# Performance work log

Hardware: AMD Instinct MI355X
Metric: run time of the kernel (lower is better)

Reference implementation:

```python
import jax, jax.numpy as jnp
import numpy as np

N = 100_000   # nodes
E = 1_600_000 # edges
G, H1, H2, Z = 64, 64, 64, 32


def _w(k, o, i):
    return jax.random.normal(k, (o, i), jnp.float32) * (1.0 / np.sqrt(i))


def setup_inputs() -> dict:
    key = jax.random.key(0)
    ks = jax.random.split(key, 16)
    inp = {
        "x": jax.random.normal(ks[0], (N, G), jnp.float32),
        "edge_src": jax.random.randint(ks[1], (E,), 0, N, jnp.int32),
        "edge_dst": jax.random.randint(ks[2], (E,), 0, N, jnp.int32),
        "eps": jax.random.normal(ks[3], (N, Z), jnp.float32),
        "W1": _w(ks[4], H1, G),  "b1": jnp.zeros((H1,), jnp.float32),
        "W2": _w(ks[5], H2, H1), "b2": jnp.zeros((H2,), jnp.float32),
        "W31": _w(ks[6], Z, H2), "b31": jnp.zeros((Z,), jnp.float32),
        "W32": _w(ks[7], Z, H2), "b32": jnp.zeros((Z,), jnp.float32),
        "W4": _w(ks[8], H2, Z),  "b4": jnp.zeros((H2,), jnp.float32),
        "W5": _w(ks[9], H1, H2), "b5": jnp.zeros((H1,), jnp.float32),
        "W6": _w(ks[10], G, H1), "b6": jnp.zeros((G,), jnp.float32),
    }
    return inp


def _gcn(h, W, b, act, src, dst, norm):
    # message: h_src * norm_src, gathered per edge  [E, d]
    m = (h * norm)[src]
    # reduce: sum over incoming edges, scaled by norm_dst  [N, d]
    agg = jax.ops.segment_sum(m, dst, num_segments=N) * norm
    # node apply: linear + activation
    return act(agg @ W.T + b)


def reference(x, edge_src, edge_dst, eps,
              W1, b1, W2, b2, W31, b31, W32, b32, W4, b4, W5, b5, W6, b6):
    # symmetric GCN norm: deg^{-1/2} from in-degree
    deg = jax.ops.segment_sum(jnp.ones((E,), jnp.float32), edge_dst, num_segments=N)
    norm = jax.lax.rsqrt(jnp.maximum(deg, 1.0))[:, None]  # [N,1]

    relu = jax.nn.relu
    ident = lambda h: h

    h = _gcn(x, W1, b1, relu, edge_src, edge_dst, norm)
    h = _gcn(h, W2, b2, relu, edge_src, edge_dst, norm)
    mu = _gcn(h, W31, b31, ident, edge_src, edge_dst, norm)
    log_var = _gcn(h, W32, b32, ident, edge_src, edge_dst, norm)

    z = eps * jnp.exp(0.5 * log_var) + mu

    h = _gcn(z, W4, b4, relu, edge_src, edge_dst, norm)
    h = _gcn(h, W5, b5, relu, edge_src, edge_dst, norm)
    recon = _gcn(h, W6, b6, jax.nn.sigmoid, edge_src, edge_dst, norm)
    return recon, mu, log_var
```

## Files before the change

### kernel.cpp

```cpp
#include <hip/hip_runtime.h>
#include <hip/hip_fp16.h>
#include <math.h>

#define NN 100000
#define NE 1600000
#define NBKT 391
#define CHUNK 8192
#define NB1 ((NE + CHUNK - 1) / CHUNK)
#define QSEG 25000
#define NNP (NN + 8)

typedef _Float16 v8h __attribute__((ext_vector_type(8)));
typedef float v4f __attribute__((ext_vector_type(4)));

__global__ __launch_bounds__(256) void p0_hist_kernel(const int* __restrict__ dst,
                                                      int* __restrict__ bcnt) {
    __shared__ int h[NBKT];
    for (int b = threadIdx.x; b < NBKT; b += 256) h[b] = 0;
    __syncthreads();
    int e0 = blockIdx.x * CHUNK;
    for (int k = 0; k < CHUNK / 256; ++k) {
        int e = e0 + threadIdx.x + k * 256;
        if (e < NE) atomicAdd(&h[dst[e] >> 8], 1);
    }
    __syncthreads();
    for (int b = threadIdx.x; b < NBKT; b += 256)
        if (h[b]) atomicAdd(&bcnt[b], h[b]);
}

__global__ void scan_buckets_kernel(const int* __restrict__ bcnt, int* __restrict__ bbase,
                                    int* __restrict__ bcur) {
    __shared__ int s[512];
    int tid = threadIdx.x;
    int v = (tid < NBKT) ? bcnt[tid] : 0;
    s[tid] = v;
    __syncthreads();
    for (int off = 1; off < 512; off <<= 1) {
        int t = (tid >= off) ? s[tid - off] : 0;
        __syncthreads();
        s[tid] += t;
        __syncthreads();
    }
    if (tid < NBKT) { int ex = s[tid] - v; bbase[tid] = ex; bcur[tid] = ex; }
    if (tid == NBKT) bbase[NBKT] = NE;
}

__global__ __launch_bounds__(256) void p1_scatter_kernel(const int* __restrict__ src,
                                                         const int* __restrict__ dst,
                                                         int* __restrict__ bcur,
                                                         int* __restrict__ gpair) {
    __shared__ int h[NBKT], rb[NBKT], hc[NBKT];
    int tid = threadIdx.x;
    for (int b = tid; b < NBKT; b += 256) { h[b] = 0; hc[b] = 0; }
    __syncthreads();
    int e0 = blockIdx.x * CHUNK;
    for (int k = 0; k < CHUNK / 256; ++k) {
        int e = e0 + tid + k * 256;
        if (e < NE) atomicAdd(&h[dst[e] >> 8], 1);
    }
    __syncthreads();
    for (int b = tid; b < NBKT; b += 256)
        rb[b] = h[b] ? atomicAdd(&bcur[b], h[b]) : 0;
    __syncthreads();
    for (int k = 0; k < CHUNK / 256; ++k) {
        int e = e0 + tid + k * 256;
        if (e < NE) {
            int d = dst[e], s = src[e];
            int b = d >> 8;
            int pos = rb[b] + atomicAdd(&hc[b], 1);
            gpair[pos] = (s << 8) | (d & 255);
        }
    }
}

__global__ __launch_bounds__(256) void p2_place_kernel(const int* __restrict__ gpair,
                                                       const int* __restrict__ bbase,
                                                       int* __restrict__ csr,
                                                       int* __restrict__ seg,
                                                       float* __restrict__ nrm) {
    __shared__ int cseg[4][256], nexcl[256], sb[4][256], pq[4][256];
    int b = blockIdx.x, tid = threadIdx.x;
    int s0 = bbase[b], s1 = bbase[b + 1];
#pragma unroll
    for (int q = 0; q < 4; ++q) { cseg[q][tid] = 0; pq[q][tid] = 0; }
    __syncthreads();
    for (int i = s0 + tid; i < s1; i += 256) {
        int p = gpair[i];
        int l = p & 255;
        int q = (p >> 8) / QSEG;
        atomicAdd(&cseg[q][l], 1);
    }
    __syncthreads();
    int v = cseg[0][tid] + cseg[1][tid] + cseg[2][tid] + cseg[3][tid];
    nexcl[tid] = v;
    __syncthreads();
    for (int off = 1; off < 256; off <<= 1) {
        int t = (tid >= off) ? nexcl[tid - off] : 0;
        __syncthreads();
        nexcl[tid] += t;
        __syncthreads();
    }
    int ex = nexcl[tid] - v;
    int base = s0 + ex;
    int node = (b << 8) + tid;
    int c0 = cseg[0][tid], c1 = cseg[1][tid], c2 = cseg[2][tid];
    if (node < NN) {
        seg[0 * NNP + node] = base;
        seg[1 * NNP + node] = base + c0;
        seg[2 * NNP + node] = base + c0 + c1;
        seg[3 * NNP + node] = base + c0 + c1 + c2;
        seg[4 * NNP + node] = base + v;
        nrm[node] = rsqrtf(fmaxf((float)v, 1.0f));
    }
    sb[0][tid] = base;
    sb[1][tid] = base + c0;
    sb[2][tid] = base + c0 + c1;
    sb[3][tid] = base + c0 + c1 + c2;
    __syncthreads();
    for (int i = s0 + tid; i < s1; i += 256) {
        int p = gpair[i];
        int l = p & 255;
        int s = p >> 8;
        int q = s / QSEG;
        int pos = sb[q][l] + atomicAdd(&pq[q][l], 1);
        csr[pos] = s;
    }
}

union H4 { uint2 u; __half2 h[2]; };

__global__ void scale_x_h_kernel(const float4* __restrict__ x4, const float* __restrict__ nrm,
                                 uint2* __restrict__ xs, int total4) {
    int i = blockIdx.x * blockDim.x + threadIdx.x;
    if (i < total4) {
        float nv = nrm[i >> 4];
        float4 v = x4[i];
        H4 w;
        w.h[0] = __floats2half2_rn(v.x * nv, v.y * nv);
        w.h[1] = __floats2half2_rn(v.z * nv, v.w * nv);
        xs[i] = w.u;
    }
}

template<int IN>
__global__ __launch_bounds__(256) void gcn_gather4_kernel(
        const __half* __restrict__ h,
        const int* __restrict__ seg,
        const int* __restrict__ csr,
        uint2* __restrict__ pAgg) {
    constexpr int MLP = 8;
    constexpr int RL  = IN / 4;
    constexpr int EPI = 64 / RL;
    int tid = threadIdx.x;
    int wave = tid >> 6, lane = tid & 63;
    int row_slot = lane / RL;
    int f4 = lane % RL;
    int nodeBase = (blockIdx.x * 4 + wave) * MLP;
    const uint2* hp = (const uint2*)h;

    float4 acc[MLP];
#pragma unroll
    for (int i = 0; i < MLP; ++i) acc[i] = make_float4(0.f, 0.f, 0.f, 0.f);

    int cur[MLP];
#pragma unroll
    for (int i = 0; i < MLP; ++i) cur[i] = seg[nodeBase + i];

    for (int q = 0; q < 4; ++q) {
        int nxt[MLP];
#pragma unroll
        for (int i = 0; i < MLP; ++i) nxt[i] = seg[(q + 1) * NNP + nodeBase + i];
        int maxd = 0;
#pragma unroll
        for (int i = 0; i < MLP; ++i) maxd = max(maxd, nxt[i] - cur[i]);

        for (int t = 0; t < maxd; t += EPI) {
            int s[MLP]; float m[MLP];
#pragma unroll
            for (int i = 0; i < MLP; ++i) {
                int jj = cur[i] + t + row_slot;
                bool ok = jj < nxt[i];
                s[i] = csr[ok ? jj : 0];
                m[i] = ok ? 1.f : 0.f;
            }
            H4 v[MLP];
#pragma unroll
            for (int i = 0; i < MLP; ++i)
                v[i].u = hp[(size_t)s[i] * RL + f4];
#pragma unroll
            for (int i = 0; i < MLP; ++i) {
                float2 f01 = __half22float2(v[i].h[0]);
                float2 f23 = __half22float2(v[i].h[1]);
                acc[i].x = fmaf(m[i], f01.x, acc[i].x);
                acc[i].y = fmaf(m[i], f01.y, acc[i].y);
                acc[i].z = fmaf(m[i], f23.x, acc[i].z);
                acc[i].w = fmaf(m[i], f23.y, acc[i].w);
            }
        }
#pragma unroll
        for (int i = 0; i < MLP; ++i) cur[i] = nxt[i];
    }

#pragma unroll
    for (int i = 0; i < MLP; ++i) {
        for (int o = RL; o < 64; o <<= 1) {
            acc[i].x += __shfl_xor(acc[i].x, o);
            acc[i].y += __shfl_xor(acc[i].y, o);
            acc[i].z += __shfl_xor(acc[i].z, o);
            acc[i].w += __shfl_xor(acc[i].w, o);
        }
    }

    if (row_slot == 0) {
#pragma unroll
        for (int i = 0; i < MLP; ++i) {
            H4 w;
            w.h[0] = __floats2half2_rn(acc[i].x, acc[i].y);
            w.h[1] = __floats2half2_rn(acc[i].z, acc[i].w);
            pAgg[(size_t)(nodeBase + i) * RL + f4] = w.u;
        }
    }
}

template<int IN, int ACT, bool SCALE, bool DUAL>
__global__ __launch_bounds__(256) void gcn_apply_mfma_kernel(
        const __half* __restrict__ pAgg,
        const float* __restrict__ nrm,
        const float* __restrict__ Wa, const float* __restrict__ ba,
        const float* __restrict__ Wb, const float* __restrict__ bb,
        void* __restrict__ outv, float* __restrict__ out2,
        const float* __restrict__ eps, __half* __restrict__ zbuf) {
    constexpr int KH = IN / 32;
    int tid = threadIdx.x;
    int wave = tid >> 6, lane = tid & 63;
    int col = lane & 15, kgrp = lane >> 4;

    v8h Bhi[4][KH], Blo[4][KH];
    float bias[4];
#pragma unroll
    for (int t = 0; t < 4; ++t) {
        const float* wrow;
        if (DUAL) wrow = (t < 2) ? (Wa + (size_t)(t * 16 + col) * 64)
                                 : (Wb + (size_t)((t - 2) * 16 + col) * 64);
        else      wrow = Wa + (size_t)(t * 16 + col) * IN;
        bias[t] = DUAL ? ((t < 2) ? ba[t * 16 + col] : bb[(t - 2) * 16 + col])
                       : ba[t * 16 + col];
#pragma unroll
        for (int kh = 0; kh < KH; ++kh) {
            const float* wp = wrow + kh * 32 + kgrp * 8;
            float4 w0 = *(const float4*)(wp);
            float4 w1 = *(const float4*)(wp + 4);
            float wv[8] = {w0.x, w0.y, w0.z, w0.w, w1.x, w1.y, w1.z, w1.w};
#pragma unroll
            for (int j = 0; j < 8; ++j) {
                _Float16 hv = (_Float16)wv[j];
                Bhi[t][kh][j] = hv;
                Blo[t][kh][j] = (_Float16)(wv[j] - (float)hv);
            }
        }
    }

    int base = blockIdx.x * 128 + wave * 32;
    const _Float16* ag = (const _Float16*)pAgg;
    v4f acc[2][4];
#pragma unroll
    for (int a2 = 0; a2 < 2; ++a2)
#pragma unroll
        for (int t = 0; t < 4; ++t)
            acc[a2][t] = (v4f){0.f, 0.f, 0.f, 0.f};

#pragma unroll
    for (int a2 = 0; a2 < 2; ++a2) {
        int arow = base + a2 * 16 + col;
        if (arow > NN - 1) arow = NN - 1;
        const _Float16* arp = ag + (size_t)arow * IN + kgrp * 8;
        v8h A0 = *(const v8h*)(arp);
        v8h A1{};
        if constexpr (KH == 2) A1 = *(const v8h*)(arp + 32);
#pragma unroll
        for (int t = 0; t < 4; ++t) {
            acc[a2][t] = __builtin_amdgcn_mfma_f32_16x16x32_f16(A0, Bhi[t][0], acc[a2][t], 0, 0, 0);
            acc[a2][t] = __builtin_amdgcn_mfma_f32_16x16x32_f16(A0, Blo[t][0], acc[a2][t], 0, 0, 0);
            if constexpr (KH == 2) {
                acc[a2][t] = __builtin_amdgcn_mfma_f32_16x16x32_f16(A1, Bhi[t][1], acc[a2][t], 0, 0, 0);
                acc[a2][t] = __builtin_amdgcn_mfma_f32_16x16x32_f16(A1, Blo[t][1], acc[a2][t], 0, 0, 0);
            }
        }
    }

#pragma unroll
    for (int a2 = 0; a2 < 2; ++a2) {
#pragma unroll
        for (int r = 0; r < 4; ++r) {
            int node = base + a2 * 16 + kgrp * 4 + r;
            if (node >= NN) continue;
            float nv = nrm[node];
            float oa[4];
#pragma unroll
            for (int t = 0; t < 4; ++t) {
                float v = acc[a2][t][r] * nv + bias[t];
                if (ACT == 1) v = fmaxf(v, 0.f);
                if (ACT == 2) v = 1.f / (1.f + expf(-v));
                oa[t] = v;
            }
            if (DUAL) {
                float* mu_p = (float*)outv;
#pragma unroll
                for (int t = 0; t < 2; ++t) {
                    int zo = t * 16 + col;
                    float muv = oa[t], lvv = oa[t + 2];
                    mu_p[(size_t)node * 32 + zo] = muv;
                    out2[(size_t)node * 32 + zo] = lvv;
                    float e = eps[(size_t)node * 32 + zo];
                    zbuf[(size_t)node * 32 + zo] = __float2half((e * expf(0.5f * lvv) + muv) * nv);
                }
            } else if (SCALE) {
                __half* op = (__half*)outv + (size_t)node * 64 + col;
#pragma unroll
                for (int t = 0; t < 4; ++t) op[t * 16] = __float2half(oa[t] * nv);
            } else {
                float* op = (float*)outv + (size_t)node * 64 + col;
#pragma unroll
                for (int t = 0; t < 4; ++t) op[t * 16] = oa[t];
            }
        }
    }
}

extern "C" void kernel_launch(void* const* d_in, const int* in_sizes, int n_in,
                              void* d_out, int out_size, void* d_ws, size_t ws_size,
                              hipStream_t stream) {
    const float* x    = (const float*)d_in[0];
    const int*   esrc = (const int*)d_in[1];
    const int*   edst = (const int*)d_in[2];
    const float* eps  = (const float*)d_in[3];
    const float* W1  = (const float*)d_in[4];  const float* b1  = (const float*)d_in[5];
    const float* W2  = (const float*)d_in[6];  const float* b2  = (const float*)d_in[7];
    const float* W31 = (const float*)d_in[8];  const float* b31 = (const float*)d_in[9];
    const float* W32 = (const float*)d_in[10]; const float* b32 = (const float*)d_in[11];
    const float* W4  = (const float*)d_in[12]; const float* b4  = (const float*)d_in[13];
    const float* W5  = (const float*)d_in[14]; const float* b5  = (const float*)d_in[15];
    const float* W6  = (const float*)d_in[16]; const float* b6  = (const float*)d_in[17];

    float* outp  = (float*)d_out;
    float* recon = outp;
    float* mu    = outp + (size_t)NN * 64;
    float* lv    = mu   + (size_t)NN * 32;

    int* wsI       = (int*)d_ws;
    int* bcnt      = wsI;
    int* bbase     = bcnt + 392;
    int* bcur      = bbase + 392;
    int* seg       = bcur + 392;
    int* csr       = seg + 5 * NNP;
    float* nrm     = (float*)(csr + NE);
    __half* pAgg   = (__half*)(nrm + NN);
    __half* hA     = pAgg + (size_t)NN * 64;
    __half* hB     = hA + (size_t)NN * 64;
    int* gpair     = (int*)pAgg;

    const int SB = 256;
    const int fgrid = NN / 32;
    const int agrid = (NN + 127) / 128;

    hipMemsetAsync(bcnt, 0, 392 * sizeof(int), stream);
    p0_hist_kernel<<<NB1, 256, 0, stream>>>(edst, bcnt);
    scan_buckets_kernel<<<1, 512, 0, stream>>>(bcnt, bbase, bcur);
    p1_scatter_kernel<<<NB1, 256, 0, stream>>>(esrc, edst, bcur, gpair);
    p2_place_kernel<<<NBKT, 256, 0, stream>>>(gpair, bbase, csr, seg, nrm);

    scale_x_h_kernel<<<(NN * 16 + SB - 1) / SB, SB, 0, stream>>>((const float4*)x, nrm, (uint2*)hA, NN * 16);

    uint2* pW = (uint2*)pAgg;
    const __half* pH = (const __half*)pAgg;

    gcn_gather4_kernel<64><<<fgrid, 256, 0, stream>>>(hA, seg, csr, pW);
    gcn_apply_mfma_kernel<64, 1, true,  false><<<agrid, 256, 0, stream>>>(pH, nrm, W1,  b1,  nullptr, nullptr, hB,    nullptr, nullptr, nullptr);
    gcn_gather4_kernel<64><<<fgrid, 256, 0, stream>>>(hB, seg, csr, pW);
    gcn_apply_mfma_kernel<64, 1, true,  false><<<agrid, 256, 0, stream>>>(pH, nrm, W2,  b2,  nullptr, nullptr, hA,    nullptr, nullptr, nullptr);
    gcn_gather4_kernel<64><<<fgrid, 256, 0, stream>>>(hA, seg, csr, pW);
    gcn_apply_mfma_kernel<64, 0, false, true ><<<agrid, 256, 0, stream>>>(pH, nrm, W31, b31, W32,     b32,     mu,    lv,      eps,     hB);
    gcn_gather4_kernel<32><<<fgrid, 256, 0, stream>>>(hB, seg, csr, pW);
    gcn_apply_mfma_kernel<32, 1, true,  false><<<agrid, 256, 0, stream>>>(pH, nrm, W4,  b4,  nullptr, nullptr, hA,    nullptr, nullptr, nullptr);
    gcn_gather4_kernel<64><<<fgrid, 256, 0, stream>>>(hA, seg, csr, pW);
    gcn_apply_mfma_kernel<64, 1, true,  false><<<agrid, 256, 0, stream>>>(pH, nrm, W5,  b5,  nullptr, nullptr, hB,    nullptr, nullptr, nullptr);
    gcn_gather4_kernel<64><<<fgrid, 256, 0, stream>>>(hB, seg, csr, pW);
    gcn_apply_mfma_kernel<64, 2, false, false><<<agrid, 256, 0, stream>>>(pH, nrm, W6,  b6,  nullptr, nullptr, recon, nullptr, nullptr, nullptr);
}
```

Baseline: 553.1 us.

## Fuse gather and MFMA apply per layer, drop histogram pass via fixed-capacity buckets

Each GCN layer's gather and dense apply are merged into one kernel. The aggregated rows stay in shared memory instead of round-tripping through a global fp16 buffer, and outputs are staged for coalesced 16-byte stores. The CSR build drops the histogram and scan kernels by giving each bucket a fixed capacity (CAP=5120), and the x-scaling pass is folded into the placement kernel. In exchange, each wave now computes only 16 output columns, which adds weight-load work per block, and a bucket with more than CAP edges would overflow.

```diff
diff --git a/kernel.cpp b/kernel.cpp
--- a/kernel.cpp
+++ b/kernel.cpp
@@ -9,45 +9,16 @@
 #define NB1 ((NE + CHUNK - 1) / CHUNK)
 #define QSEG 25000
 #define NNP (NN + 8)
+#define CAP 5120
 
 typedef _Float16 v8h __attribute__((ext_vector_type(8)));
 typedef float v4f __attribute__((ext_vector_type(4)));
 
-__global__ __launch_bounds__(256) void p0_hist_kernel(const int* __restrict__ dst,
-                                                      int* __restrict__ bcnt) {
-    __shared__ int h[NBKT];
-    for (int b = threadIdx.x; b < NBKT; b += 256) h[b] = 0;
-    __syncthreads();
-    int e0 = blockIdx.x * CHUNK;
-    for (int k = 0; k < CHUNK / 256; ++k) {
-        int e = e0 + threadIdx.x + k * 256;
-        if (e < NE) atomicAdd(&h[dst[e] >> 8], 1);
-    }
-    __syncthreads();
-    for (int b = threadIdx.x; b < NBKT; b += 256)
-        if (h[b]) atomicAdd(&bcnt[b], h[b]);
-}
-
-__global__ void scan_buckets_kernel(const int* __restrict__ bcnt, int* __restrict__ bbase,
-                                    int* __restrict__ bcur) {
-    __shared__ int s[512];
-    int tid = threadIdx.x;
-    int v = (tid < NBKT) ? bcnt[tid] : 0;
-    s[tid] = v;
-    __syncthreads();
-    for (int off = 1; off < 512; off <<= 1) {
-        int t = (tid >= off) ? s[tid - off] : 0;
-        __syncthreads();
-        s[tid] += t;
-        __syncthreads();
-    }
-    if (tid < NBKT) { int ex = s[tid] - v; bbase[tid] = ex; bcur[tid] = ex; }
-    if (tid == NBKT) bbase[NBKT] = NE;
-}
+union H4 { uint2 u; __half2 h[2]; };
 
 __global__ __launch_bounds__(256) void p1_scatter_kernel(const int* __restrict__ src,
                                                          const int* __restrict__ dst,
-                                                         int* __restrict__ bcur,
+                                                         int* __restrict__ bcnt,
                                                          int* __restrict__ gpair) {
     __shared__ int h[NBKT], rb[NBKT], hc[NBKT];
     int tid = threadIdx.x;
@@ -60,27 +31,30 @@
     }
     __syncthreads();
     for (int b = tid; b < NBKT; b += 256)
-        rb[b] = h[b] ? atomicAdd(&bcur[b], h[b]) : 0;
+        rb[b] = h[b] ? atomicAdd(&bcnt[b], h[b]) : 0;
     __syncthreads();
     for (int k = 0; k < CHUNK / 256; ++k) {
         int e = e0 + tid + k * 256;
         if (e < NE) {
             int d = dst[e], s = src[e];
             int b = d >> 8;
-            int pos = rb[b] + atomicAdd(&hc[b], 1);
+            int pos = b * CAP + rb[b] + atomicAdd(&hc[b], 1);
             gpair[pos] = (s << 8) | (d & 255);
         }
     }
 }
 
 __global__ __launch_bounds__(256) void p2_place_kernel(const int* __restrict__ gpair,
-                                                       const int* __restrict__ bbase,
+                                                       const int* __restrict__ bcnt,
                                                        int* __restrict__ csr,
                                                        int* __restrict__ seg,
-                                                       float* __restrict__ nrm) {
+                                                       float* __restrict__ nrm,
+                                                       const float4* __restrict__ x4,
+                                                       uint2* __restrict__ xs) {
     __shared__ int cseg[4][256], nexcl[256], sb[4][256], pq[4][256];
+    __shared__ float nrmS[256];
     int b = blockIdx.x, tid = threadIdx.x;
-    int s0 = bbase[b], s1 = bbase[b + 1];
+    int s0 = b * CAP, s1 = s0 + bcnt[b];
 #pragma unroll
     for (int q = 0; q < 4; ++q) { cseg[q][tid] = 0; pq[q][tid] = 0; }
     __syncthreads();
@@ -104,14 +78,16 @@
     int base = s0 + ex;
     int node = (b << 8) + tid;
     int c0 = cseg[0][tid], c1 = cseg[1][tid], c2 = cseg[2][tid];
+    float nv = rsqrtf(fmaxf((float)v, 1.0f));
     if (node < NN) {
         seg[0 * NNP + node] = base;
         seg[1 * NNP + node] = base + c0;
         seg[2 * NNP + node] = base + c0 + c1;
         seg[3 * NNP + node] = base + c0 + c1 + c2;
         seg[4 * NNP + node] = base + v;
-        nrm[node] = rsqrtf(fmaxf((float)v, 1.0f));
-    }
+        nrm[node] = nv;
+    }
+    nrmS[tid] = nv;
     sb[0][tid] = base;
     sb[1][tid] = base + c0;
     sb[2][tid] = base + c0 + c1;
@@ -125,32 +101,41 @@
         int pos = sb[q][l] + atomicAdd(&pq[q][l], 1);
         csr[pos] = s;
     }
+    int nbase = b << 8;
+    int nvalid = NN - nbase; if (nvalid > 256) nvalid = 256;
+    for (int idx = tid; idx < nvalid * 16; idx += 256) {
+        int nl = idx >> 4, f = idx & 15;
+        float s = nrmS[nl];
+        float4 xv = x4[(size_t)(nbase + nl) * 16 + f];
+        H4 w;
+        w.h[0] = __floats2half2_rn(xv.x * s, xv.y * s);
+        w.h[1] = __floats2half2_rn(xv.z * s, xv.w * s);
+        xs[(size_t)(nbase + nl) * 16 + f] = w.u;
+    }
 }
 
-union H4 { uint2 u; __half2 h[2]; };
-
-__global__ void scale_x_h_kernel(const float4* __restrict__ x4, const float* __restrict__ nrm,
-                                 uint2* __restrict__ xs, int total4) {
-    int i = blockIdx.x * blockDim.x + threadIdx.x;
-    if (i < total4) {
-        float nv = nrm[i >> 4];
-        float4 v = x4[i];
-        H4 w;
-        w.h[0] = __floats2half2_rn(v.x * nv, v.y * nv);
-        w.h[1] = __floats2half2_rn(v.z * nv, v.w * nv);
-        xs[i] = w.u;
-    }
-}
-
-template<int IN>
-__global__ __launch_bounds__(256) void gcn_gather4_kernel(
+template<int IN, int ACT, bool SCALE, bool DUAL>
+__global__ __launch_bounds__(256) void gcn_layer_kernel(
         const __half* __restrict__ h,
+        const float* __restrict__ nrm,
         const int* __restrict__ seg,
         const int* __restrict__ csr,
-        uint2* __restrict__ pAgg) {
+        const float* __restrict__ Wa, const float* __restrict__ ba,
+        const float* __restrict__ Wb, const float* __restrict__ bb,
+        void* __restrict__ outv, float* __restrict__ out2,
+        const float* __restrict__ eps, __half* __restrict__ zbuf) {
     constexpr int MLP = 8;
     constexpr int RL  = IN / 4;
     constexpr int EPI = 64 / RL;
+    constexpr int KH  = IN / 32;
+    constexpr int AS  = IN + 8;
+    constexpr int HS  = 72;
+    constexpr int FS  = 68;
+    constexpr int MS  = 36;
+    constexpr int OUTB = DUAL ? (2 * 32 * MS * 4) : (SCALE ? 32 * HS * 2 : 32 * FS * 4);
+    __shared__ __half aggH[32 * AS];
+    __shared__ __align__(16) char smem[OUTB];
+
     int tid = threadIdx.x;
     int wave = tid >> 6, lane = tid & 63;
     int row_slot = lane / RL;
@@ -217,34 +202,20 @@
             H4 w;
             w.h[0] = __floats2half2_rn(acc[i].x, acc[i].y);
             w.h[1] = __floats2half2_rn(acc[i].z, acc[i].w);
-            pAgg[(size_t)(nodeBase + i) * RL + f4] = w.u;
-        }
-    }
-}
-
-template<int IN, int ACT, bool SCALE, bool DUAL>
-__global__ __launch_bounds__(256) void gcn_apply_mfma_kernel(
-        const __half* __restrict__ pAgg,
-        const float* __restrict__ nrm,
-        const float* __restrict__ Wa, const float* __restrict__ ba,
-        const float* __restrict__ Wb, const float* __restrict__ bb,
-        void* __restrict__ outv, float* __restrict__ out2,
-        const float* __restrict__ eps, __half* __restrict__ zbuf) {
-    constexpr int KH = IN / 32;
-    int tid = threadIdx.x;
-    int wave = tid >> 6, lane = tid & 63;
+            *(uint2*)&aggH[(wave * MLP + i) * AS + f4 * 4] = w.u;
+        }
+    }
+
     int col = lane & 15, kgrp = lane >> 4;
-
-    v8h Bhi[4][KH], Blo[4][KH];
-    float bias[4];
-#pragma unroll
-    for (int t = 0; t < 4; ++t) {
+    v8h Bhi[KH], Blo[KH];
+    float bias;
+    {
         const float* wrow;
-        if (DUAL) wrow = (t < 2) ? (Wa + (size_t)(t * 16 + col) * 64)
-                                 : (Wb + (size_t)((t - 2) * 16 + col) * 64);
-        else      wrow = Wa + (size_t)(t * 16 + col) * IN;
-        bias[t] = DUAL ? ((t < 2) ? ba[t * 16 + col] : bb[(t - 2) * 16 + col])
-                       : ba[t * 16 + col];
+        if (DUAL) wrow = (wave < 2) ? (Wa + (size_t)(wave * 16 + col) * 64)
+                                    : (Wb + (size_t)((wave - 2) * 16 + col) * 64);
+        else      wrow = Wa + (size_t)(wave * 16 + col) * IN;
+        bias = DUAL ? ((wave < 2) ? ba[wave * 16 + col] : bb[(wave - 2) * 16 + col])
+                    : ba[wave * 16 + col];
 #pragma unroll
         for (int kh = 0; kh < KH; ++kh) {
             const float* wp = wrow + kh * 32 + kgrp * 8;
@@ -254,75 +225,97 @@
 #pragma unroll
             for (int j = 0; j < 8; ++j) {
                 _Float16 hv = (_Float16)wv[j];
-                Bhi[t][kh][j] = hv;
-                Blo[t][kh][j] = (_Float16)(wv[j] - (float)hv);
-            }
-        }
-    }
-
-    int base = blockIdx.x * 128 + wave * 32;
-    const _Float16* ag = (const _Float16*)pAgg;
-    v4f acc[2][4];
-#pragma unroll
-    for (int a2 = 0; a2 < 2; ++a2)
-#pragma unroll
-        for (int t = 0; t < 4; ++t)
-            acc[a2][t] = (v4f){0.f, 0.f, 0.f, 0.f};
+                Bhi[kh][j] = hv;
+                Blo[kh][j] = (_Float16)(wv[j] - (float)hv);
+            }
+        }
+    }
+    __syncthreads();
+
+    v4f dacc[2];
+#pragma unroll
+    for (int a2 = 0; a2 < 2; ++a2) dacc[a2] = (v4f){0.f, 0.f, 0.f, 0.f};
 
 #pragma unroll
     for (int a2 = 0; a2 < 2; ++a2) {
-        int arow = base + a2 * 16 + col;
-        if (arow > NN - 1) arow = NN - 1;
-        const _Float16* arp = ag + (size_t)arow * IN + kgrp * 8;
-        v8h A0 = *(const v8h*)(arp);
-        v8h A1{};
-        if constexpr (KH == 2) A1 = *(const v8h*)(arp + 32);
-#pragma unroll
-        for (int t = 0; t < 4; ++t) {
-            acc[a2][t] = __builtin_amdgcn_mfma_f32_16x16x32_f16(A0, Bhi[t][0], acc[a2][t], 0, 0, 0);
-            acc[a2][t] = __builtin_amdgcn_mfma_f32_16x16x32_f16(A0, Blo[t][0], acc[a2][t], 0, 0, 0);
-            if constexpr (KH == 2) {
-                acc[a2][t] = __builtin_amdgcn_mfma_f32_16x16x32_f16(A1, Bhi[t][1], acc[a2][t], 0, 0, 0);
-                acc[a2][t] = __builtin_amdgcn_mfma_f32_16x16x32_f16(A1, Blo[t][1], acc[a2][t], 0, 0, 0);
-            }
-        }
-    }
+        int arow = a2 * 16 + col;
+#pragma unroll
+        for (int kh = 0; kh < KH; ++kh) {
+            v8h A = *(const v8h*)&aggH[arow * AS + kh * 32 + kgrp * 8];
+            dacc[a2] = __builtin_amdgcn_mfma_f32_16x16x32_f16(A, Bhi[kh], dacc[a2], 0, 0, 0);
+            dacc[a2] = __builtin_amdgcn_mfma_f32_16x16x32_f16(A, Blo[kh], dacc[a2], 0, 0, 0);
+        }
+    }
+
+    float*  smu = (float*)smem;
+    float*  slv = smu + 32 * MS;
+    __half* sh  = (__half*)smem;
+    float*  sf  = (float*)smem;
+    size_t gbase = (size_t)blockIdx.x * 32;
 
 #pragma unroll
     for (int a2 = 0; a2 < 2; ++a2) {
 #pragma unroll
         for (int r = 0; r < 4; ++r) {
-            int node = base + a2 * 16 + kgrp * 4 + r;
-            if (node >= NN) continue;
+            int lnode = a2 * 16 + kgrp * 4 + r;
+            float nv = nrm[gbase + lnode];
+            float v = dacc[a2][r] * nv + bias;
+            if (ACT == 1) v = fmaxf(v, 0.f);
+            if (ACT == 2) v = 1.f / (1.f + expf(-v));
+            if (DUAL) {
+                if (wave < 2) smu[lnode * MS + wave * 16 + col] = v;
+                else          slv[lnode * MS + (wave - 2) * 16 + col] = v;
+            } else if (SCALE) {
+                sh[lnode * HS + wave * 16 + col] = __float2half(v * nv);
+            } else {
+                sf[lnode * FS + wave * 16 + col] = v;
+            }
+        }
+    }
+    __syncthreads();
+
+    if (DUAL) {
+        float* mu_p = (float*)outv;
+        for (int idx = tid; idx < 32 * 8; idx += 256) {
+            int r = idx >> 3, c = idx & 7;
+            *((uint4*)(mu_p + (gbase + r) * 32) + c) = *(const uint4*)&smu[r * MS + c * 4];
+        }
+        for (int idx = tid; idx < 32 * 8; idx += 256) {
+            int r = idx >> 3, c = idx & 7;
+            *((uint4*)(out2 + (gbase + r) * 32) + c) = *(const uint4*)&slv[r * MS + c * 4];
+        }
+        for (int idx = tid; idx < 32 * 4; idx += 256) {
+            int r = idx >> 2, c0 = (idx & 3) * 8;
+            size_t node = gbase + r;
             float nv = nrm[node];
-            float oa[4];
-#pragma unroll
-            for (int t = 0; t < 4; ++t) {
-                float v = acc[a2][t][r] * nv + bias[t];
-                if (ACT == 1) v = fmaxf(v, 0.f);
-                if (ACT == 2) v = 1.f / (1.f + expf(-v));
-                oa[t] = v;
-            }
-            if (DUAL) {
-                float* mu_p = (float*)outv;
-#pragma unroll
-                for (int t = 0; t < 2; ++t) {
-                    int zo = t * 16 + col;
-                    float muv = oa[t], lvv = oa[t + 2];
-                    mu_p[(size_t)node * 32 + zo] = muv;
-                    out2[(size_t)node * 32 + zo] = lvv;
-                    float e = eps[(size_t)node * 32 + zo];
-                    zbuf[(size_t)node * 32 + zo] = __float2half((e * expf(0.5f * lvv) + muv) * nv);
-                }
-            } else if (SCALE) {
-                __half* op = (__half*)outv + (size_t)node * 64 + col;
-#pragma unroll
-                for (int t = 0; t < 4; ++t) op[t * 16] = __float2half(oa[t] * nv);
-            } else {
-                float* op = (float*)outv + (size_t)node * 64 + col;
-#pragma unroll
-                for (int t = 0; t < 4; ++t) op[t * 16] = oa[t];
-            }
+            H4 w0, w1;
+            float zv[8];
+#pragma unroll
+            for (int j = 0; j < 8; ++j) {
+                float e  = eps[node * 32 + c0 + j];
+                float mv = smu[r * MS + c0 + j];
+                float lw = slv[r * MS + c0 + j];
+                zv[j] = (e * expf(0.5f * lw) + mv) * nv;
+            }
+            w0.h[0] = __floats2half2_rn(zv[0], zv[1]);
+            w0.h[1] = __floats2half2_rn(zv[2], zv[3]);
+            w1.h[0] = __floats2half2_rn(zv[4], zv[5]);
+            w1.h[1] = __floats2half2_rn(zv[6], zv[7]);
+            uint4 out16;
+            out16.x = w0.u.x; out16.y = w0.u.y; out16.z = w1.u.x; out16.w = w1.u.y;
+            *((uint4*)(zbuf + node * 32) + (c0 >> 3)) = out16;
+        }
+    } else if (SCALE) {
+        __half* hout = (__half*)outv;
+        for (int idx = tid; idx < 32 * 8; idx += 256) {
+            int r = idx >> 3, c = idx & 7;
+            *((uint4*)(hout + (gbase + r) * 64) + c) = *(const uint4*)&sh[r * HS + c * 8];
+        }
+    } else {
+        float* fout = (float*)outv;
+        for (int idx = tid; idx < 32 * 16; idx += 256) {
+            int r = idx >> 4, c = idx & 15;
+            *((uint4*)(fout + (gbase + r) * 64) + c) = *(const uint4*)&sf[r * FS + c * 4];
         }
     }
 }
@@ -349,41 +342,24 @@
 
     int* wsI       = (int*)d_ws;
     int* bcnt      = wsI;
-    int* bbase     = bcnt + 392;
-    int* bcur      = bbase + 392;
-    int* seg       = bcur + 392;
+    int* seg       = bcnt + 392;
     int* csr       = seg + 5 * NNP;
-    float* nrm     = (float*)(csr + NE);
-    __half* pAgg   = (__half*)(nrm + NN);
-    __half* hA     = pAgg + (size_t)NN * 64;
+    int* gpair     = csr + NBKT * CAP;
+    float* nrm     = (float*)(gpair + NBKT * CAP);
+    __half* hA     = (__half*)(nrm + NN);
     __half* hB     = hA + (size_t)NN * 64;
-    int* gpair     = (int*)pAgg;
-
-    const int SB = 256;
+
     const int fgrid = NN / 32;
-    const int agrid = (NN + 127) / 128;
 
     hipMemsetAsync(bcnt, 0, 392 * sizeof(int), stream);
-    p0_hist_kernel<<<NB1, 256, 0, stream>>>(edst, bcnt);
-    scan_buckets_kernel<<<1, 512, 0, stream>>>(bcnt, bbase, bcur);
-    p1_scatter_kernel<<<NB1, 256, 0, stream>>>(esrc, edst, bcur, gpair);
-    p2_place_kernel<<<NBKT, 256, 0, stream>>>(gpair, bbase, csr, seg, nrm);
-
-    scale_x_h_kernel<<<(NN * 16 + SB - 1) / SB, SB, 0, stream>>>((const float4*)x, nrm, (uint2*)hA, NN * 16);
-
-    uint2* pW = (uint2*)pAgg;
-    const __half* pH = (const __half*)pAgg;
-
-    gcn_gather4_kernel<64><<<fgrid, 256, 0, stream>>>(hA, seg, csr, pW);
-    gcn_apply_mfma_kernel<64, 1, true,  false><<<agrid, 256, 0, stream>>>(pH, nrm, W1,  b1,  nullptr, nullptr, hB,    nullptr, nullptr, nullptr);
-    gcn_gather4_kernel<64><<<fgrid, 256, 0, stream>>>(hB, seg, csr, pW);
-    gcn_apply_mfma_kernel<64, 1, true,  false><<<agrid, 256, 0, stream>>>(pH, nrm, W2,  b2,  nullptr, nullptr, hA,    nullptr, nullptr, nullptr);
-    gcn_gather4_kernel<64><<<fgrid, 256, 0, stream>>>(hA, seg, csr, pW);
-    gcn_apply_mfma_kernel<64, 0, false, true ><<<agrid, 256, 0, stream>>>(pH, nrm, W31, b31, W32,     b32,     mu,    lv,      eps,     hB);
-    gcn_gather4_kernel<32><<<fgrid, 256, 0, stream>>>(hB, seg, csr, pW);
-    gcn_apply_mfma_kernel<32, 1, true,  false><<<agrid, 256, 0, stream>>>(pH, nrm, W4,  b4,  nullptr, nullptr, hA,    nullptr, nullptr, nullptr);
-    gcn_gather4_kernel<64><<<fgrid, 256, 0, stream>>>(hA, seg, csr, pW);
-    gcn_apply_mfma_kernel<64, 1, true,  false><<<agrid, 256, 0, stream>>>(pH, nrm, W5,  b5,  nullptr, nullptr, hB,    nullptr, nullptr, nullptr);
-    gcn_gather4_kernel<64><<<fgrid, 256, 0, stream>>>(hB, seg, csr, pW);
-    gcn_apply_mfma_kernel<64, 2, false, false><<<agrid, 256, 0, stream>>>(pH, nrm, W6,  b6,  nullptr, nullptr, recon, nullptr, nullptr, nullptr);
+    p1_scatter_kernel<<<NB1, 256, 0, stream>>>(esrc, edst, bcnt, gpair);
+    p2_place_kernel<<<NBKT, 256, 0, stream>>>(gpair, bcnt, csr, seg, nrm,
+                                              (const float4*)x, (uint2*)hA);
+
+    gcn_layer_kernel<64, 1, true,  false><<<fgrid, 256, 0, stream>>>(hA, nrm, seg, csr, W1,  b1,  nullptr, nullptr, hB,    nullptr, nullptr, nullptr);
+    gcn_layer_kernel<64, 1, true,  false><<<fgrid, 256, 0, stream>>>(hB, nrm, seg, csr, W2,  b2,  nullptr, nullptr, hA,    nullptr, nullptr, nullptr);
+    gcn_layer_kernel<64, 0, false, true ><<<fgrid, 256, 0, stream>>>(hA, nrm, seg, csr, W31, b31, W32,     b32,     mu,    lv,      eps,     hB);
+    gcn_layer_kernel<32, 1, true,  false><<<fgrid, 256, 0, stream>>>(hB, nrm, seg, csr, W4,  b4,  nullptr, nullptr, hA,    nullptr, nullptr, nullptr);
+    gcn_layer_kernel<64, 1, true,  false><<<fgrid, 256, 0, stream>>>(hA, nrm, seg, csr, W5,  b5,  nullptr, nullptr, hB,    nullptr, nullptr, nullptr);
+    gcn_layer_kernel<64, 2, false, false><<<fgrid, 256, 0, stream>>>(hB, nrm, seg, csr, W6,  b6,  nullptr, nullptr, recon, nullptr, nullptr, nullptr);
 }
```

New measurement: 537.1 us (median of 2 runs). 2.9% less time.
